# Kernel tuning notes

Measured on AMD Instinct MI355X. Metric: run time of the kernel, lower is better.

## Reference

```python
import jax, jax.numpy as jnp
import numpy as np

N_SRC = 100000
N_DST = 100000
E = 1600000
OUT = 64

def setup_inputs() -> dict:
    key = jax.random.key(0)
    ks = jax.random.split(key, 9)
    return {
        'weight': jax.random.normal(ks[0], (N_SRC, OUT), dtype=jnp.float32) * 0.05,
        'prob_w': jax.random.normal(ks[1], (1, OUT), dtype=jnp.float32) * 0.1,
        'review_score_w': jax.random.normal(ks[2], (1, OUT), dtype=jnp.float32) * 0.1,
        'review_w': jax.random.normal(ks[3], (OUT, OUT), dtype=jnp.float32) * 0.1,
        'review_feat': jax.random.normal(ks[4], (E, OUT), dtype=jnp.float32),
        'cj': jax.random.uniform(ks[5], (N_SRC, 1), dtype=jnp.float32),
        'ci': jax.random.uniform(ks[6], (N_DST, 1), dtype=jnp.float32),
        'src_idx': jax.random.randint(ks[7], (E,), 0, N_SRC, dtype=jnp.int32),
        'dst_idx': jax.random.randint(ks[8], (E,), 0, N_DST, dtype=jnp.int32),
    }

def reference(weight, prob_w, review_score_w, review_w, review_feat, cj, ci, src_idx, dst_idx):
    # Edge-wise gates from review features
    pa = jax.nn.sigmoid(review_feat @ prob_w.T)                         # [E, 1]
    rf = (review_feat @ review_w.T) * jax.nn.sigmoid(review_feat @ review_score_w.T)  # [E, OUT]
    # Gather src node feats (weight rows) and cj norm, form messages
    m = (weight[src_idx] * pa + rf) * cj[src_idx]                       # [E, OUT] (dropout_rate=0 -> identity)
    # Scatter-sum to dst nodes, then scale by ci
    h = jax.ops.segment_sum(m, dst_idx, num_segments=N_DST)             # [N_DST, OUT]
    return h * ci
```

## Files before the change

### kernel.cpp

```cpp
#include <hip/hip_runtime.h>

typedef __attribute__((ext_vector_type(8))) short short8;
typedef __attribute__((ext_vector_type(16))) float f32x16;

union Frag { short8 v; unsigned u[4]; };

__device__ __forceinline__ unsigned pack_bf16(float lo, float hi) {
    unsigned r;
    asm volatile("v_cvt_pk_bf16_f32 %0, %1, %2" : "=v"(r) : "v"(lo), "v"(hi));
    return r;
}

#define BSHIFT 6
#define BROWS 64
#define MAXNB 2048
#define CHUNK 8192

__global__ __launch_bounds__(256)
void k_hist(const int* __restrict__ dst, int* __restrict__ ghist, int E, int NB) {
    __shared__ int h[MAXNB];
    const int tid = threadIdx.x;
    for (int b = tid; b < NB; b += 256) h[b] = 0;
    __syncthreads();
    const int c0 = blockIdx.x * CHUNK;
    const int c1 = min(c0 + CHUNK, E);
    for (int i = c0 + tid; i < c1; i += 256) atomicAdd(&h[dst[i] >> BSHIFT], 1);
    __syncthreads();
    for (int b = tid; b < NB; b += 256) {
        const int cnt = h[b];
        if (cnt) atomicAdd(&ghist[b], cnt);
    }
}

__global__ __launch_bounds__(512)
void k_scan(const int* __restrict__ ghist, int* __restrict__ gcursor,
            int* __restrict__ gbase, int NB, int E) {
    __shared__ int wsum[8];
    const int tid = threadIdx.x, lane = tid & 63, wv = tid >> 6;
    const int i0 = tid * 4;
    const int4 v = *reinterpret_cast<const int4*>(ghist + i0);
    const int s0 = v.x, s1 = s0 + v.y, s2 = s1 + v.z, s3 = s2 + v.w;
    int s = s3;
#pragma unroll
    for (int off = 1; off < 64; off <<= 1) {
        const int t = __shfl_up(s, off, 64);
        if (lane >= off) s += t;
    }
    if (lane == 63) wsum[wv] = s;
    __syncthreads();
    int wbase = 0;
    for (int w = 0; w < wv; ++w) wbase += wsum[w];
    const int tb = wbase + s - s3;
    if (i0 + 0 < NB) { gcursor[i0 + 0] = tb;      gbase[i0 + 0] = tb; }
    if (i0 + 1 < NB) { gcursor[i0 + 1] = tb + s0; gbase[i0 + 1] = tb + s0; }
    if (i0 + 2 < NB) { gcursor[i0 + 2] = tb + s1; gbase[i0 + 2] = tb + s1; }
    if (i0 + 3 < NB) { gcursor[i0 + 3] = tb + s2; gbase[i0 + 3] = tb + s2; }
    if (tid == 0) gbase[NB] = E;
}

__global__ __launch_bounds__(256)
void k_scatter(const int* __restrict__ src, const int* __restrict__ dst,
               int* __restrict__ gcursor, int2* __restrict__ recs, int E, int NB) {
    __shared__ int cur[MAXNB];
    const int tid = threadIdx.x;
    for (int b = tid; b < NB; b += 256) cur[b] = 0;
    __syncthreads();
    const int c0 = blockIdx.x * CHUNK;
    const int c1 = min(c0 + CHUNK, E);
    for (int i = c0 + tid; i < c1; i += 256) atomicAdd(&cur[dst[i] >> BSHIFT], 1);
    __syncthreads();
    for (int b = tid; b < NB; b += 256) {
        const int cnt = cur[b];
        if (cnt) cur[b] = atomicAdd(&gcursor[b], cnt);
    }
    __syncthreads();
    for (int i = c0 + tid; i < c1; i += 256) {
        const int d = dst[i];
        const int slot = atomicAdd(&cur[d >> BSHIFT], 1);
        recs[slot] = make_int2(i, (src[i] & 0xFFFFF) | ((d & (BROWS - 1)) << 20));
    }
}

__global__ __launch_bounds__(256)
void k_sortbucket(const int2* __restrict__ recs, const int* __restrict__ gbase,
                  int2* __restrict__ recsS) {
    __shared__ int bins[BROWS];
    const int tid = threadIdx.x;
    const int lane = tid & 63;
    const int b = blockIdx.x;
    const int start = gbase[b], end = gbase[b + 1];
    const int n = end - start;
    if (tid < BROWS) bins[tid] = 0;
    __syncthreads();
    for (int i = tid; i < n; i += 256)
        atomicAdd(&bins[(recs[start + i].y >> 20) & (BROWS - 1)], 1);
    __syncthreads();
    if (tid < BROWS) {
        const int v = bins[tid];
        int s = v;
#pragma unroll
        for (int off = 1; off < 64; off <<= 1) {
            const int t = __shfl_up(s, off, 64);
            if (lane >= off) s += t;
        }
        bins[tid] = s - v;
    }
    __syncthreads();
    for (int i = tid; i < n; i += 256) {
        const int2 r = recs[start + i];
        const int dl = (r.y >> 20) & (BROWS - 1);
        const int slot = start + atomicAdd(&bins[dl], 1);
        recsS[slot] = make_int2(r.x | (dl << 21), (r.y & 0xFFFFF) | (b << 20));
    }
}

__device__ __forceinline__ void batch_body(
    int eid, int se, int d, float cjci, const Frag bf[2][4],
    const float4* __restrict__ pw4, const float4* __restrict__ sw4,
    const float4* __restrict__ ft4,
    const float* __restrict__ weight, float* __restrict__ out,
    int h, int c, int& prev_d, float& r0acc, float& r1acc)
{
    Frag af[4];
    float px = 0.0f, sx = 0.0f;
#pragma unroll
    for (int s = 0; s < 4; ++s) {
        const size_t base = (size_t)eid * 16 + 4 * s + 2 * h;
        const float4 f0 = ft4[base];
        const float4 f1 = ft4[base + 1];
        const float4 p0 = pw4[4 * s + 2 * h];
        const float4 p1 = pw4[4 * s + 2 * h + 1];
        const float4 q0 = sw4[4 * s + 2 * h];
        const float4 q1 = sw4[4 * s + 2 * h + 1];
        px += f0.x * p0.x + f0.y * p0.y + f0.z * p0.z + f0.w * p0.w
            + f1.x * p1.x + f1.y * p1.y + f1.z * p1.z + f1.w * p1.w;
        sx += f0.x * q0.x + f0.y * q0.y + f0.z * q0.z + f0.w * q0.w
            + f1.x * q1.x + f1.y * q1.y + f1.z * q1.z + f1.w * q1.w;
        af[s].u[0] = pack_bf16(f0.x, f0.y);
        af[s].u[1] = pack_bf16(f0.z, f0.w);
        af[s].u[2] = pack_bf16(f1.x, f1.y);
        af[s].u[3] = pack_bf16(f1.z, f1.w);
    }
    px += __shfl_xor(px, 32, 64);
    sx += __shfl_xor(sx, 32, 64);
    const float pa = __fdividef(1.0f, 1.0f + __expf(-px));
    const float gs = __fdividef(1.0f, 1.0f + __expf(-sx));
    const float Ae = pa * cjci;
    const float Be = gs * cjci;

    f32x16 acc0 = {0.0f};
    f32x16 acc1 = {0.0f};
#pragma unroll
    for (int s = 0; s < 4; ++s) {
        acc0 = __builtin_amdgcn_mfma_f32_32x32x16_bf16(af[s].v, bf[0][s].v, acc0, 0, 0, 0);
        acc1 = __builtin_amdgcn_mfma_f32_32x32x16_bf16(af[s].v, bf[1][s].v, acc1, 0, 0, 0);
    }
#pragma unroll
    for (int r = 0; r < 16; ++r) {
        const int e_lr = (r & 3) + 8 * (r >> 2) + 4 * h;
        const float Ar = __shfl(Ae, e_lr, 64);
        const float Br = __shfl(Be, e_lr, 64);
        const int sr = __shfl(se, e_lr, 64);
        const int dr = __shfl(d, e_lr, 64);
        const float w0 = weight[sr * 64 + c];
        const float w1 = weight[sr * 64 + 32 + c];
        const float m0 = acc0[r] * Br + w0 * Ar;
        const float m1 = acc1[r] * Br + w1 * Ar;
        if (__any(dr != prev_d)) {
            if (dr != prev_d) {
                if (prev_d >= 0) {
                    unsafeAtomicAdd(&out[(size_t)prev_d * 64 + c], r0acc);
                    unsafeAtomicAdd(&out[(size_t)prev_d * 64 + 32 + c], r1acc);
                }
                r0acc = 0.0f; r1acc = 0.0f; prev_d = dr;
            }
        }
        r0acc += m0;
        r1acc += m1;
    }
}

__global__ __launch_bounds__(256, 2)
void k_main(const float* __restrict__ weight, const float* __restrict__ prob_w,
            const float* __restrict__ rscore_w, const float* __restrict__ review_w,
            const float* __restrict__ feat, const float* __restrict__ cj,
            const float* __restrict__ ci,
            const int2* __restrict__ recsS, float* __restrict__ out, int E)
{
    const int lane = threadIdx.x & 63;
    const int h = lane >> 5;
    const int c = lane & 31;
    const int wid = blockIdx.x * (blockDim.x >> 6) + (threadIdx.x >> 6);
    const int nw = gridDim.x * (blockDim.x >> 6);

    const float4* rw4 = reinterpret_cast<const float4*>(review_w);
    const float4* pw4 = reinterpret_cast<const float4*>(prob_w);
    const float4* sw4 = reinterpret_cast<const float4*>(rscore_w);
    const float4* ft4 = reinterpret_cast<const float4*>(feat);

    Frag bf[2][4];
#pragma unroll
    for (int t = 0; t < 2; ++t) {
#pragma unroll
        for (int s = 0; s < 4; ++s) {
            const float4 r0 = rw4[(32 * t + c) * 16 + 4 * s + 2 * h];
            const float4 r1 = rw4[(32 * t + c) * 16 + 4 * s + 2 * h + 1];
            bf[t][s].u[0] = pack_bf16(r0.x, r0.y);
            bf[t][s].u[1] = pack_bf16(r0.z, r0.w);
            bf[t][s].u[2] = pack_bf16(r1.x, r1.y);
            bf[t][s].u[3] = pack_bf16(r1.z, r1.w);
        }
    }

    const int nbt = (E + 31) >> 5;
    const int q = nbt / nw, rr = nbt % nw;
    const int bt0 = wid * q + min(wid, rr);
    const int bt1 = bt0 + q + (wid < rr ? 1 : 0);

    int prev_d = -1;
    float r0acc = 0.0f, r1acc = 0.0f;
    for (int bt = bt0; bt < bt1; ++bt) {
        const int idx = (bt << 5) + c;
        const bool valid = idx < E;
        const int2 rec = recsS[min(idx, E - 1)];
        const int eid = rec.x & 0x1FFFFF;
        const int dl = (rec.x >> 21) & (BROWS - 1);
        const int se = rec.y & 0xFFFFF;
        const int bkt = (int)(((unsigned)rec.y) >> 20);
        const int d = (bkt << BSHIFT) | dl;
        const float cjci = valid ? cj[se] * ci[d] : 0.0f;

        float w0a[16], w1a[16];
#pragma unroll
        for (int r = 0; r < 16; ++r) {
            const int e_lr = (r & 3) + 8 * (r >> 2) + 4 * h;
            const int sr = __shfl(se, e_lr, 64);
            w0a[r] = weight[sr * 64 + c];
            w1a[r] = weight[sr * 64 + 32 + c];
        }

        Frag af[4];
        float px = 0.0f, sx = 0.0f;
#pragma unroll
        for (int s = 0; s < 4; ++s) {
            const size_t base = (size_t)eid * 16 + 4 * s + 2 * h;
            const float4 f0 = ft4[base];
            const float4 f1 = ft4[base + 1];
            const float4 p0 = pw4[4 * s + 2 * h];
            const float4 p1 = pw4[4 * s + 2 * h + 1];
            const float4 q0 = sw4[4 * s + 2 * h];
            const float4 q1 = sw4[4 * s + 2 * h + 1];
            px += f0.x * p0.x + f0.y * p0.y + f0.z * p0.z + f0.w * p0.w
                + f1.x * p1.x + f1.y * p1.y + f1.z * p1.z + f1.w * p1.w;
            sx += f0.x * q0.x + f0.y * q0.y + f0.z * q0.z + f0.w * q0.w
                + f1.x * q1.x + f1.y * q1.y + f1.z * q1.z + f1.w * q1.w;
            af[s].u[0] = pack_bf16(f0.x, f0.y);
            af[s].u[1] = pack_bf16(f0.z, f0.w);
            af[s].u[2] = pack_bf16(f1.x, f1.y);
            af[s].u[3] = pack_bf16(f1.z, f1.w);
        }
        px += __shfl_xor(px, 32, 64);
        sx += __shfl_xor(sx, 32, 64);
        const float pa = __fdividef(1.0f, 1.0f + __expf(-px));
        const float gs = __fdividef(1.0f, 1.0f + __expf(-sx));
        const float Ae = pa * cjci;
        const float Be = gs * cjci;

        f32x16 acc0 = {0.0f};
        f32x16 acc1 = {0.0f};
#pragma unroll
        for (int s = 0; s < 4; ++s) {
            acc0 = __builtin_amdgcn_mfma_f32_32x32x16_bf16(af[s].v, bf[0][s].v, acc0, 0, 0, 0);
            acc1 = __builtin_amdgcn_mfma_f32_32x32x16_bf16(af[s].v, bf[1][s].v, acc1, 0, 0, 0);
        }

#pragma unroll
        for (int r = 0; r < 16; ++r) {
            const int e_lr = (r & 3) + 8 * (r >> 2) + 4 * h;
            const float Ar = __shfl(Ae, e_lr, 64);
            const float Br = __shfl(Be, e_lr, 64);
            const int dr = __shfl(d, e_lr, 64);
            const float m0 = acc0[r] * Br + w0a[r] * Ar;
            const float m1 = acc1[r] * Br + w1a[r] * Ar;
            if (__any(dr != prev_d)) {
                if (dr != prev_d) {
                    if (prev_d >= 0) {
                        unsafeAtomicAdd(&out[(size_t)prev_d * 64 + c], r0acc);
                        unsafeAtomicAdd(&out[(size_t)prev_d * 64 + 32 + c], r1acc);
                    }
                    r0acc = 0.0f; r1acc = 0.0f; prev_d = dr;
                }
            }
            r0acc += m0;
            r1acc += m1;
        }
    }
    if (prev_d >= 0) {
        unsafeAtomicAdd(&out[(size_t)prev_d * 64 + c], r0acc);
        unsafeAtomicAdd(&out[(size_t)prev_d * 64 + 32 + c], r1acc);
    }
}

__global__ __launch_bounds__(256, 2)
void k_direct(const float* __restrict__ weight, const float* __restrict__ prob_w,
              const float* __restrict__ rscore_w, const float* __restrict__ review_w,
              const float* __restrict__ feat, const float* __restrict__ cj,
              const float* __restrict__ ci, const int* __restrict__ src_idx,
              const int* __restrict__ dst_idx, float* __restrict__ out, int E)
{
    const int lane = threadIdx.x & 63;
    const int h = lane >> 5, c = lane & 31;
    const int wid = blockIdx.x * (blockDim.x >> 6) + (threadIdx.x >> 6);
    const int nw = gridDim.x * (blockDim.x >> 6);
    const float4* rw4 = reinterpret_cast<const float4*>(review_w);
    const float4* pw4 = reinterpret_cast<const float4*>(prob_w);
    const float4* sw4 = reinterpret_cast<const float4*>(rscore_w);
    const float4* ft4 = reinterpret_cast<const float4*>(feat);
    Frag bf[2][4];
#pragma unroll
    for (int t = 0; t < 2; ++t)
#pragma unroll
        for (int s = 0; s < 4; ++s) {
            const float4 r0 = rw4[(32 * t + c) * 16 + 4 * s + 2 * h];
            const float4 r1 = rw4[(32 * t + c) * 16 + 4 * s + 2 * h + 1];
            bf[t][s].u[0] = pack_bf16(r0.x, r0.y);
            bf[t][s].u[1] = pack_bf16(r0.z, r0.w);
            bf[t][s].u[2] = pack_bf16(r1.x, r1.y);
            bf[t][s].u[3] = pack_bf16(r1.z, r1.w);
        }
    const int ntot = (E + 31) >> 5;
    for (int bt = wid; bt < ntot; bt += nw) {
        const int idx = (bt << 5) + c;
        const bool valid = idx < E;
        const int eid = valid ? idx : 0;
        const int se = src_idx[eid];
        const int d = dst_idx[eid];
        const float cjci = valid ? cj[se] * ci[d] : 0.0f;
        int pd = -1;
        float a0 = 0.0f, a1 = 0.0f;
        batch_body(eid, se, d, cjci, bf, pw4, sw4, ft4, weight, out,
                   h, c, pd, a0, a1);
        if (pd >= 0) {
            unsafeAtomicAdd(&out[(size_t)pd * 64 + c], a0);
            unsafeAtomicAdd(&out[(size_t)pd * 64 + 32 + c], a1);
        }
    }
}

extern "C" void kernel_launch(void* const* d_in, const int* in_sizes, int n_in,
                              void* d_out, int out_size, void* d_ws, size_t ws_size,
                              hipStream_t stream) {
    const float* weight    = (const float*)d_in[0];
    const float* prob_w    = (const float*)d_in[1];
    const float* rscore_w  = (const float*)d_in[2];
    const float* review_w  = (const float*)d_in[3];
    const float* feat      = (const float*)d_in[4];
    const float* cj        = (const float*)d_in[5];
    const float* ci        = (const float*)d_in[6];
    const int*   src_idx   = (const int*)d_in[7];
    const int*   dst_idx   = (const int*)d_in[8];
    float* out = (float*)d_out;
    const int E = in_sizes[7];
    const int N_DST = in_sizes[6];
    const int N_SRC = in_sizes[0] / 64;
    const int NB = (N_DST + BROWS - 1) >> BSHIFT;

    hipMemsetAsync(d_out, 0, (size_t)out_size * sizeof(float), stream);

    const size_t rec_off = 32768;
    const size_t need = rec_off + 2 * (size_t)E * sizeof(int2);
    if (ws_size < need || NB > MAXNB - 1 || N_SRC > (1 << 20) || E > (1 << 21)) {
        k_direct<<<2048, 256, 0, stream>>>(weight, prob_w, rscore_w, review_w, feat,
                                           cj, ci, src_idx, dst_idx, out, E);
        return;
    }
    int* ghist   = (int*)d_ws;
    int* gcursor = ghist + 2048;
    int* gbase   = ghist + 4096;
    int2* recs   = (int2*)((char*)d_ws + rec_off);
    int2* recsS  = recs + E;

    hipMemsetAsync(ghist, 0, 2048 * sizeof(int), stream);

    const int nchunk = (E + CHUNK - 1) / CHUNK;
    k_hist<<<nchunk, 256, 0, stream>>>(dst_idx, ghist, E, NB);
    k_scan<<<1, 512, 0, stream>>>(ghist, gcursor, gbase, NB, E);
    k_scatter<<<nchunk, 256, 0, stream>>>(src_idx, dst_idx, gcursor, recs, E, NB);
    k_sortbucket<<<NB, 256, 0, stream>>>(recs, gbase, recsS);
    k_main<<<2048, 256, 0, stream>>>(weight, prob_w, rscore_w, review_w, feat,
                                     cj, ci, recsS, out, E);
}
```

Baseline: 268.7 us.

## Convert gathered weight table to bf16 and load edge records directly per row

Adds a pre-pass kernel that converts the fp32 weight table to bf16 in the workspace. The main kernel then gathers 2-byte rows instead of 4-byte rows, halving gather traffic. It also reloads each record from recsS per accumulator row instead of shuffling src and dst indices across lanes. The cost is an extra conversion pass over the 25.6 MB table each call, plus bf16 rounding of the weight term, which changes numerics.

Measured after the change: 279.7 us. 1.04x slower.

```diff
diff --git a/kernel.cpp b/kernel.cpp
--- a/kernel.cpp
+++ b/kernel.cpp
@@ -15,6 +15,22 @@
 #define BROWS 64
 #define MAXNB 2048
 #define CHUNK 8192
+
+__global__ __launch_bounds__(256)
+void k_wconv(const float* __restrict__ w, unsigned short* __restrict__ wb, int n) {
+    int i = (blockIdx.x * 256 + threadIdx.x) * 4;
+    const int stride = gridDim.x * 1024;
+    for (; i + 3 < n; i += stride) {
+        const float4 v = *reinterpret_cast<const float4*>(w + i);
+        ushort4 o;
+        unsigned a;
+        a = __float_as_uint(v.x); o.x = (unsigned short)((a + 0x7FFF + ((a >> 16) & 1)) >> 16);
+        a = __float_as_uint(v.y); o.y = (unsigned short)((a + 0x7FFF + ((a >> 16) & 1)) >> 16);
+        a = __float_as_uint(v.z); o.z = (unsigned short)((a + 0x7FFF + ((a >> 16) & 1)) >> 16);
+        a = __float_as_uint(v.w); o.w = (unsigned short)((a + 0x7FFF + ((a >> 16) & 1)) >> 16);
+        *reinterpret_cast<ushort4*>(wb + i) = o;
+    }
+}
 
 __global__ __launch_bounds__(256)
 void k_hist(const int* __restrict__ dst, int* __restrict__ ghist, int E, int NB) {
@@ -181,7 +197,7 @@
 }
 
 __global__ __launch_bounds__(256, 2)
-void k_main(const float* __restrict__ weight, const float* __restrict__ prob_w,
+void k_main(const unsigned short* __restrict__ weightB, const float* __restrict__ prob_w,
             const float* __restrict__ rscore_w, const float* __restrict__ review_w,
             const float* __restrict__ feat, const float* __restrict__ cj,
             const float* __restrict__ ci,
@@ -230,13 +246,18 @@
         const int d = (bkt << BSHIFT) | dl;
         const float cjci = valid ? cj[se] * ci[d] : 0.0f;
 
-        float w0a[16], w1a[16];
+        unsigned wp[16];
+        int dra[16];
 #pragma unroll
         for (int r = 0; r < 16; ++r) {
             const int e_lr = (r & 3) + 8 * (r >> 2) + 4 * h;
-            const int sr = __shfl(se, e_lr, 64);
-            w0a[r] = weight[sr * 64 + c];
-            w1a[r] = weight[sr * 64 + 32 + c];
+            const int2 rrc = recsS[min((bt << 5) + e_lr, E - 1)];
+            const int sr = rrc.y & 0xFFFFF;
+            dra[r] = (int)(((((unsigned)rrc.y) >> 20) << BSHIFT) |
+                           (unsigned)((rrc.x >> 21) & (BROWS - 1)));
+            const unsigned u0 = weightB[sr * 64 + c];
+            const unsigned u1 = weightB[sr * 64 + 32 + c];
+            wp[r] = u0 | (u1 << 16);
         }
 
         Frag af[4];
@@ -279,9 +300,11 @@
             const int e_lr = (r & 3) + 8 * (r >> 2) + 4 * h;
             const float Ar = __shfl(Ae, e_lr, 64);
             const float Br = __shfl(Be, e_lr, 64);
-            const int dr = __shfl(d, e_lr, 64);
-            const float m0 = acc0[r] * Br + w0a[r] * Ar;
-            const float m1 = acc1[r] * Br + w1a[r] * Ar;
+            const int dr = dra[r];
+            const float w0 = __uint_as_float((wp[r] & 0xFFFFu) << 16);
+            const float w1 = __uint_as_float(wp[r] & 0xFFFF0000u);
+            const float m0 = acc0[r] * Br + w0 * Ar;
+            const float m1 = acc1[r] * Br + w1 * Ar;
             if (__any(dr != prev_d)) {
                 if (dr != prev_d) {
                     if (prev_d >= 0) {
@@ -368,7 +391,8 @@
     hipMemsetAsync(d_out, 0, (size_t)out_size * sizeof(float), stream);
 
     const size_t rec_off = 32768;
-    const size_t need = rec_off + 2 * (size_t)E * sizeof(int2);
+    const size_t wb_off = rec_off + 2 * (size_t)E * sizeof(int2);
+    const size_t need = wb_off + (size_t)N_SRC * 64 * sizeof(unsigned short);
     if (ws_size < need || NB > MAXNB - 1 || N_SRC > (1 << 20) || E > (1 << 21)) {
         k_direct<<<2048, 256, 0, stream>>>(weight, prob_w, rscore_w, review_w, feat,
                                            cj, ci, src_idx, dst_idx, out, E);
@@ -379,14 +403,16 @@
     int* gbase   = ghist + 4096;
     int2* recs   = (int2*)((char*)d_ws + rec_off);
     int2* recsS  = recs + E;
+    unsigned short* weightB = (unsigned short*)((char*)d_ws + wb_off);
 
     hipMemsetAsync(ghist, 0, 2048 * sizeof(int), stream);
 
     const int nchunk = (E + CHUNK - 1) / CHUNK;
+    k_wconv<<<1024, 256, 0, stream>>>(weight, weightB, N_SRC * 64);
     k_hist<<<nchunk, 256, 0, stream>>>(dst_idx, ghist, E, NB);
     k_scan<<<1, 512, 0, stream>>>(ghist, gcursor, gbase, NB, E);
     k_scatter<<<nchunk, 256, 0, stream>>>(src_idx, dst_idx, gcursor, recs, E, NB);
     k_sortbucket<<<NB, 256, 0, stream>>>(recs, gbase, recsS);
-    k_main<<<2048, 256, 0, stream>>>(weight, prob_w, rscore_w, review_w, feat,
+    k_main<<<2048, 256, 0, stream>>>(weightB, prob_w, rscore_w, review_w, feat,
                                      cj, ci, recsS, out, E);
 }
```
